# Kernel optimization log

Measured on AMD Instinct MI355X. Metric: run time of the kernel, lower is better.

The kernel has to match this reference:

```python
import jax, jax.numpy as jnp
import numpy as np

N, T, H, KQ, V = 8, 256, 8, 128, 32  # batch, seq (Tq=Tk=T), heads, kq_dim, value_dim(=latent_dim)
SCALE = 1.0 / np.sqrt(KQ)


def setup_inputs() -> dict:
    k = jax.random.split(jax.random.key(0), 10)
    w = 0.05
    return {
        "value": jax.random.normal(k[0], (N, T, V), dtype=jnp.float32),
        "key": jax.random.normal(k[1], (N, T, KQ), dtype=jnp.float32),
        "query": jax.random.normal(k[2], (N, T, KQ), dtype=jnp.float32),
        "mask": jax.random.randint(k[3], (N, T, V), 0, 2, dtype=jnp.int32),
        # attn_linear[0]: query proj, attn_linear[1]: key proj (torch Linear: y = x @ W.T + b)
        "Wq": jax.random.normal(k[4], (H * KQ, KQ), dtype=jnp.float32) * w,
        "bq": jax.random.normal(k[5], (H * KQ,), dtype=jnp.float32) * w,
        "Wk": jax.random.normal(k[6], (H * KQ, KQ), dtype=jnp.float32) * w,
        "bk": jax.random.normal(k[7], (H * KQ,), dtype=jnp.float32) * w,
        "Wo": jax.random.normal(k[8], (V, H * V), dtype=jnp.float32) * w,  # attn_out: Linear(ld*H, ld), ld == V
        "bo": jax.random.normal(k[9], (V,), dtype=jnp.float32) * w,
    }


def reference(value, key, query, mask, Wq, bq, Wk, bk, Wo, bo):
    n, t, vdim = value.shape
    nq, tq, _ = query.shape
    nk, tk, _ = key.shape
    h = Wq.shape[0] // query.shape[-1]
    kq = query.shape[-1]

    # per-head projections: (N, H, T, KQ)
    hq = (query @ Wq.T + bq).reshape(nq, tq, h, kq).transpose(0, 2, 1, 3)
    hk = (key @ Wk.T + bk).reshape(nk, tk, h, kq).transpose(0, 2, 1, 3)

    # scores: (N, H, Tq, Tk), then broadcast per value-dim -> (N, H, Tq, Tk, V)
    scores = jnp.einsum("nhqd,nhkd->nhqk", hq, hk) * jnp.asarray(SCALE, value.dtype)
    scores = jnp.broadcast_to(scores[..., None], (n, h, tq, tk, vdim))

    # mask (N, Tk, V): mask[i,t,d]==0 means value[i,t,d] unobserved
    m = mask[:, None, None, :, :]  # (N,1,1,Tk,V)
    scores = jnp.where(m == 0, jnp.asarray(-1e9, scores.dtype), scores)

    p_attn = jax.nn.softmax(scores, axis=-2)  # softmax over Tk, per value-dim

    # weighted sum over keys: (N, H, Tq, V) -> (N, Tq, H*V)
    out = jnp.einsum("nhqkv,nkv->nqhv", p_attn, value).reshape(n, tq, h * vdim)
    out_rep = out @ Wo.T + bo  # (N, Tq, ld)
    return out_rep, p_attn
```

## Files before the change

### kernel.cpp

```cpp
#include <hip/hip_runtime.h>

#define N_ 8
#define T_ 256
#define H_ 8
#define KQ_ 128
#define V_ 32
#define QT_ 8

typedef float f32x4 __attribute__((ext_vector_type(4)));

__global__ __launch_bounds__(256) void proj_kernel(
    const float* __restrict__ query, const float* __restrict__ key,
    const float* __restrict__ Wq, const float* __restrict__ bq,
    const float* __restrict__ Wk, const float* __restrict__ bk,
    float* __restrict__ hqT, float* __restrict__ hkT)
{
  int b = blockIdx.x;
  int dh = b & 1;
  int tq = (b >> 1) & 3;
  int h  = (b >> 3) & 7;
  int n  = (b >> 6) & 7;
  int proj = b >> 9;
  const float* src  = proj ? key : query;
  const float* W    = proj ? Wk  : Wq;
  const float* bias = proj ? bk  : bq;
  float* dst        = proj ? hkT : hqT;
  int t0 = tq * 64;
  int d0 = dh * 64;

  __shared__ float qs[64 * 132];
  __shared__ float ws[64 * 128];

  {
    const float* qsrc = src + ((size_t)n * T_ + t0) * KQ_;
    const float* wsrc = W + (size_t)(h * KQ_ + d0) * KQ_;
    for (int i = threadIdx.x; i < 64 * 32; i += 256) {
      int r = i >> 5, c4 = (i & 31) * 4;
      *(float4*)&qs[r * 132 + c4] = *(const float4*)&qsrc[(size_t)r * KQ_ + c4];
      *(float4*)&ws[r * 128 + c4] = *(const float4*)&wsrc[(size_t)r * KQ_ + c4];
    }
  }
  __syncthreads();

  int tl   = threadIdx.x & 31;
  int dsub = threadIdx.x >> 5;
  float acc0[8], acc1[8];
#pragma unroll
  for (int dd = 0; dd < 8; ++dd) { acc0[dd] = 0.f; acc1[dd] = 0.f; }

#pragma unroll 4
  for (int j0 = 0; j0 < 128; j0 += 4) {
    float4 q0 = *(const float4*)&qs[tl * 132 + j0];
    float4 q1 = *(const float4*)&qs[(tl + 32) * 132 + j0];
#pragma unroll
    for (int dd = 0; dd < 8; ++dd) {
      float4 w4 = *(const float4*)&ws[(dsub * 8 + dd) * 128 + j0];
      acc0[dd] = fmaf(q0.x, w4.x, acc0[dd]);
      acc0[dd] = fmaf(q0.y, w4.y, acc0[dd]);
      acc0[dd] = fmaf(q0.z, w4.z, acc0[dd]);
      acc0[dd] = fmaf(q0.w, w4.w, acc0[dd]);
      acc1[dd] = fmaf(q1.x, w4.x, acc1[dd]);
      acc1[dd] = fmaf(q1.y, w4.y, acc1[dd]);
      acc1[dd] = fmaf(q1.z, w4.z, acc1[dd]);
      acc1[dd] = fmaf(q1.w, w4.w, acc1[dd]);
    }
  }

#pragma unroll
  for (int dd = 0; dd < 8; ++dd) {
    int d = d0 + dsub * 8 + dd;
    float bb = bias[h * KQ_ + d];
    size_t base = (((size_t)n * H_ + h) * KQ_ + d) * T_ + t0;
    dst[base + tl]      = acc0[dd] + bb;
    dst[base + tl + 32] = acc1[dd] + bb;
  }
}

#define EPAD 9

__global__ __launch_bounds__(256) void attn_kernel(
    const float* __restrict__ hqT, const float* __restrict__ hkT,
    const int* __restrict__ mask, const float* __restrict__ value,
    float* __restrict__ e_ws, float* __restrict__ inv_ws,
    float* __restrict__ out_ws)
{
  const float SCALE = 0.08838834764831845f;
  int b = blockIdx.x;
  int q0 = (b & 31) * QT_;
  int h  = (b >> 5) & 7;
  int n  = b >> 8;
  int t  = threadIdx.x;
  int row0 = (n * H_ + h) * T_ + q0;

  __shared__ float hq_s[KQ_ * 8];
  __shared__ float e_s[T_ * EPAD];
  __shared__ float wred[4 * 8];
  __shared__ float red_s[8 * 8 * 32];
  __shared__ float red_o[8 * 8 * 32];

  const float* hqbase = hqT + ((size_t)n * H_ + h) * KQ_ * T_;
  const float* hkbase = hkT + ((size_t)n * H_ + h) * KQ_ * T_;

  {
    int qq = t & 7, j0 = t >> 3;
#pragma unroll
    for (int rep = 0; rep < 4; ++rep) {
      int j = j0 + rep * 32;
      hq_s[j * 8 + qq] = hqbase[(size_t)j * T_ + q0 + qq];
    }
  }
  __syncthreads();

  float acc[8];
#pragma unroll
  for (int qq = 0; qq < 8; ++qq) acc[qq] = 0.f;
#pragma unroll 4
  for (int j = 0; j < KQ_; ++j) {
    float hk = hkbase[(size_t)j * T_ + t];
    float4 a0 = *(const float4*)&hq_s[j * 8];
    float4 a1 = *(const float4*)&hq_s[j * 8 + 4];
    acc[0] = fmaf(a0.x, hk, acc[0]);
    acc[1] = fmaf(a0.y, hk, acc[1]);
    acc[2] = fmaf(a0.z, hk, acc[2]);
    acc[3] = fmaf(a0.w, hk, acc[3]);
    acc[4] = fmaf(a1.x, hk, acc[4]);
    acc[5] = fmaf(a1.y, hk, acc[5]);
    acc[6] = fmaf(a1.z, hk, acc[6]);
    acc[7] = fmaf(a1.w, hk, acc[7]);
  }
#pragma unroll
  for (int qq = 0; qq < 8; ++qq) acc[qq] *= SCALE;

  float mloc[8];
#pragma unroll
  for (int qq = 0; qq < 8; ++qq) {
    float m = acc[qq];
    for (int off = 32; off >= 1; off >>= 1)
      m = fmaxf(m, __shfl_xor(m, off, 64));
    mloc[qq] = m;
  }
  if ((t & 63) == 0) {
    int w = t >> 6;
#pragma unroll
    for (int qq = 0; qq < 8; ++qq) wred[w * 8 + qq] = mloc[qq];
  }
  __syncthreads();
  {
    float ev[8];
#pragma unroll
    for (int qq = 0; qq < 8; ++qq) {
      float mx = fmaxf(fmaxf(wred[0*8+qq], wred[1*8+qq]),
                       fmaxf(wred[2*8+qq], wred[3*8+qq]));
      ev[qq] = __expf(acc[qq] - mx);
    }
    *(float4*)&e_s[t * EPAD]     = make_float4(ev[0], ev[1], ev[2], ev[3]);
    *(float4*)&e_s[t * EPAD + 4] = make_float4(ev[4], ev[5], ev[6], ev[7]);
#pragma unroll
    for (int qq = 0; qq < 8; ++qq)
      e_ws[(size_t)(row0 + qq) * T_ + t] = ev[qq];
  }
  __syncthreads();

  const int*   mrow = mask  + (size_t)n * T_ * V_;
  const float* vrow = value + (size_t)n * T_ * V_;
  int v = t & 31, kg = t >> 5;
  float s8[8], o8[8];
#pragma unroll
  for (int qq = 0; qq < 8; ++qq) { s8[qq] = 0.f; o8[qq] = 0.f; }
  for (int i = 0; i < 32; ++i) {
    int k = kg * 32 + i;
    float mf = (float)mrow[k * V_ + v];
    float vv = vrow[k * V_ + v];
    float4 e0 = *(const float4*)&e_s[k * EPAD];
    float4 e1 = *(const float4*)&e_s[k * EPAD + 4];
    float p;
    p = e0.x * mf; s8[0] += p; o8[0] = fmaf(p, vv, o8[0]);
    p = e0.y * mf; s8[1] += p; o8[1] = fmaf(p, vv, o8[1]);
    p = e0.z * mf; s8[2] += p; o8[2] = fmaf(p, vv, o8[2]);
    p = e0.w * mf; s8[3] += p; o8[3] = fmaf(p, vv, o8[3]);
    p = e1.x * mf; s8[4] += p; o8[4] = fmaf(p, vv, o8[4]);
    p = e1.y * mf; s8[5] += p; o8[5] = fmaf(p, vv, o8[5]);
    p = e1.z * mf; s8[6] += p; o8[6] = fmaf(p, vv, o8[6]);
    p = e1.w * mf; s8[7] += p; o8[7] = fmaf(p, vv, o8[7]);
  }
#pragma unroll
  for (int qq = 0; qq < 8; ++qq) {
    red_s[(kg * 8 + qq) * 32 + v] = s8[qq];
    red_o[(kg * 8 + qq) * 32 + v] = o8[qq];
  }
  __syncthreads();
  {
    int qq = t >> 5, v2 = t & 31;
    float s = 0.f, o = 0.f;
#pragma unroll
    for (int kg2 = 0; kg2 < 8; ++kg2) {
      s += red_s[(kg2 * 8 + qq) * 32 + v2];
      o += red_o[(kg2 * 8 + qq) * 32 + v2];
    }
    float inv = 1.0f / s;
    inv_ws[(size_t)(row0 + qq) * V_ + v2] = inv;
    out_ws[(((size_t)n * T_ + q0 + qq) * H_ + h) * V_ + v2] = o * inv;
  }
}

__global__ __launch_bounds__(256) void pwrite_kernel(
    const float* __restrict__ e_ws, const float* __restrict__ inv_ws,
    const int* __restrict__ mask, float* __restrict__ p_out)
{
  int b = blockIdx.x;
  int row0 = b * 4;
  int n = row0 >> 11;
  const int* mrow = mask + (size_t)n * T_ * V_;
  int t = threadIdx.x;
  int v0 = (t & 7) * 4;
  int kbase = t >> 3;

  float4 iv[4];
  const float* erow[4];
  f32x4* dst4[4];
#pragma unroll
  for (int qq = 0; qq < 4; ++qq) {
    int row = row0 + qq;
    iv[qq]   = *(const float4*)&inv_ws[(size_t)row * V_ + v0];
    erow[qq] = e_ws + (size_t)row * T_;
    dst4[qq] = (f32x4*)p_out + (size_t)row * 2048;
  }

#pragma unroll
  for (int rep = 0; rep < 8; ++rep) {
    int k = rep * 32 + kbase;
    const int4 m4 = *(const int4*)&mrow[k * V_ + v0];
    float fx = (float)m4.x, fy = (float)m4.y, fz = (float)m4.z, fw = (float)m4.w;
#pragma unroll
    for (int qq = 0; qq < 4; ++qq) {
      float e = erow[qq][k];
      f32x4 pv;
      pv.x = e * fx * iv[qq].x;
      pv.y = e * fy * iv[qq].y;
      pv.z = e * fz * iv[qq].z;
      pv.w = e * fw * iv[qq].w;
      __builtin_nontemporal_store(pv, &dst4[qq][rep * 256 + t]);
    }
  }
}

__global__ __launch_bounds__(256) void outproj_kernel(
    const float* __restrict__ out_ws, const float* __restrict__ Wo,
    const float* __restrict__ bo, float* __restrict__ out_rep)
{
  __shared__ float wot[256 * 33];
  __shared__ float rows_s[4 * 256];
  __shared__ float red[4 * 32];
  int r0 = blockIdx.x * 4;
  for (int i = threadIdx.x; i < 32 * 256; i += 256) {
    int o = i >> 8, c = i & 255;
    wot[c * 33 + o] = Wo[i];
  }
  for (int i = threadIdx.x; i < 4 * 256; i += 256)
    rows_s[i] = out_ws[(size_t)r0 * 256 + i];
  __syncthreads();
  int o  = threadIdx.x & 31;
  int rr = (threadIdx.x >> 5) & 3;
  int kh = threadIdx.x >> 7;
  int cb = kh * 128;
  float acc = 0.f;
#pragma unroll 4
  for (int c = 0; c < 128; ++c)
    acc = fmaf(rows_s[rr * 256 + cb + c], wot[(cb + c) * 33 + o], acc);
  if (kh == 1) red[rr * 32 + o] = acc;
  __syncthreads();
  if (kh == 0)
    out_rep[(size_t)(r0 + rr) * 32 + o] = acc + red[rr * 32 + o] + bo[o];
}

extern "C" void kernel_launch(void* const* d_in, const int* in_sizes, int n_in,
                              void* d_out, int out_size, void* d_ws, size_t ws_size,
                              hipStream_t stream) {
  const float* value = (const float*)d_in[0];
  const float* key   = (const float*)d_in[1];
  const float* query = (const float*)d_in[2];
  const int*   mask  = (const int*)d_in[3];
  const float* Wq = (const float*)d_in[4];
  const float* bq = (const float*)d_in[5];
  const float* Wk = (const float*)d_in[6];
  const float* bk = (const float*)d_in[7];
  const float* Wo = (const float*)d_in[8];
  const float* bo = (const float*)d_in[9];

  float* out_rep = (float*)d_out;
  float* p_out   = (float*)d_out + (size_t)N_ * T_ * V_;

  float* hqT    = (float*)d_ws;
  float* hkT    = hqT    + (size_t)N_ * H_ * KQ_ * T_;
  float* out_ws = hkT    + (size_t)N_ * H_ * KQ_ * T_;
  float* e_ws   = out_ws + (size_t)N_ * T_ * H_ * V_;
  float* inv_ws = e_ws   + (size_t)N_ * H_ * T_ * T_;

  hipLaunchKernelGGL(proj_kernel, dim3(1024), dim3(256), 0, stream,
                     query, key, Wq, bq, Wk, bk, hqT, hkT);
  hipLaunchKernelGGL(attn_kernel, dim3(2048), dim3(256), 0, stream,
                     hqT, hkT, mask, value, e_ws, inv_ws, out_ws);
  hipLaunchKernelGGL(pwrite_kernel, dim3(4096), dim3(256), 0, stream,
                     e_ws, inv_ws, mask, p_out);
  hipLaunchKernelGGL(outproj_kernel, dim3(512), dim3(256), 0, stream,
                     out_ws, Wo, bo, out_rep);
}
```

Before: 170.4 us.

## Retile projection to full sequence per block and shrink attention blocks to one wavefront

The projection kernel now has each block cover all 256 tokens for a 64-wide output slice, looping over K in 32-wide chunks with an 8x8 register tile per thread. This quarters the block count and reuses each weight tile across the whole sequence. The attention kernel now runs one 64-thread wavefront per block, with each lane handling four keys. The softmax max and the final reductions use wave shuffles instead of shared-memory reductions and block barriers. The trade-off is less parallelism: 256 projection blocks and 2048 single-wave attention blocks, plus higher register pressure that may reduce occupancy.

```diff
diff --git a/kernel.cpp b/kernel.cpp
--- a/kernel.cpp
+++ b/kernel.cpp
@@ -5,7 +5,6 @@
 #define H_ 8
 #define KQ_ 128
 #define V_ 32
-#define QT_ 8
 
 typedef float f32x4 __attribute__((ext_vector_type(4)));
 
@@ -17,52 +16,65 @@
 {
   int b = blockIdx.x;
   int dh = b & 1;
-  int tq = (b >> 1) & 3;
-  int h  = (b >> 3) & 7;
-  int n  = (b >> 6) & 7;
-  int proj = b >> 9;
+  int h  = (b >> 1) & 7;
+  int n  = (b >> 4) & 7;
+  int proj = (b >> 7) & 1;
   const float* src  = proj ? key : query;
   const float* W    = proj ? Wk  : Wq;
   const float* bias = proj ? bk  : bq;
   float* dst        = proj ? hkT : hqT;
-  int t0 = tq * 64;
   int d0 = dh * 64;
 
-  __shared__ float qs[64 * 132];
-  __shared__ float ws[64 * 128];
-
-  {
-    const float* qsrc = src + ((size_t)n * T_ + t0) * KQ_;
-    const float* wsrc = W + (size_t)(h * KQ_ + d0) * KQ_;
-    for (int i = threadIdx.x; i < 64 * 32; i += 256) {
-      int r = i >> 5, c4 = (i & 31) * 4;
-      *(float4*)&qs[r * 132 + c4] = *(const float4*)&qsrc[(size_t)r * KQ_ + c4];
-      *(float4*)&ws[r * 128 + c4] = *(const float4*)&wsrc[(size_t)r * KQ_ + c4];
-    }
-  }
-  __syncthreads();
+  __shared__ float qs[256 * 36];
+  __shared__ float ws[64 * 36];
 
   int tl   = threadIdx.x & 31;
   int dsub = threadIdx.x >> 5;
-  float acc0[8], acc1[8];
-#pragma unroll
-  for (int dd = 0; dd < 8; ++dd) { acc0[dd] = 0.f; acc1[dd] = 0.f; }
-
-#pragma unroll 4
-  for (int j0 = 0; j0 < 128; j0 += 4) {
-    float4 q0 = *(const float4*)&qs[tl * 132 + j0];
-    float4 q1 = *(const float4*)&qs[(tl + 32) * 132 + j0];
-#pragma unroll
-    for (int dd = 0; dd < 8; ++dd) {
-      float4 w4 = *(const float4*)&ws[(dsub * 8 + dd) * 128 + j0];
-      acc0[dd] = fmaf(q0.x, w4.x, acc0[dd]);
-      acc0[dd] = fmaf(q0.y, w4.y, acc0[dd]);
-      acc0[dd] = fmaf(q0.z, w4.z, acc0[dd]);
-      acc0[dd] = fmaf(q0.w, w4.w, acc0[dd]);
-      acc1[dd] = fmaf(q1.x, w4.x, acc1[dd]);
-      acc1[dd] = fmaf(q1.y, w4.y, acc1[dd]);
-      acc1[dd] = fmaf(q1.z, w4.z, acc1[dd]);
-      acc1[dd] = fmaf(q1.w, w4.w, acc1[dd]);
+  const float* qsrc = src + (size_t)n * T_ * KQ_;
+  const float* wsrc = W + (size_t)(h * KQ_ + d0) * KQ_;
+
+  float acc[8][8];
+#pragma unroll
+  for (int it = 0; it < 8; ++it)
+#pragma unroll
+    for (int dd = 0; dd < 8; ++dd) acc[it][dd] = 0.f;
+
+  for (int kc = 0; kc < 4; ++kc) {
+    if (kc) __syncthreads();
+    {
+      int r = threadIdx.x >> 3, c4 = (threadIdx.x & 7) * 4;
+#pragma unroll
+      for (int rep = 0; rep < 8; ++rep) {
+        int row = r + rep * 32;
+        *(float4*)&qs[row * 36 + c4] =
+            *(const float4*)&qsrc[(size_t)row * KQ_ + kc * 32 + c4];
+      }
+#pragma unroll
+      for (int rep = 0; rep < 2; ++rep) {
+        int row = r + rep * 32;
+        *(float4*)&ws[row * 36 + c4] =
+            *(const float4*)&wsrc[(size_t)row * KQ_ + kc * 32 + c4];
+      }
+    }
+    __syncthreads();
+
+#pragma unroll 2
+    for (int j0 = 0; j0 < 32; j0 += 4) {
+      float4 qv[8];
+#pragma unroll
+      for (int it = 0; it < 8; ++it)
+        qv[it] = *(const float4*)&qs[(tl + 32 * it) * 36 + j0];
+#pragma unroll
+      for (int dd = 0; dd < 8; ++dd) {
+        float4 w4 = *(const float4*)&ws[(dsub * 8 + dd) * 36 + j0];
+#pragma unroll
+        for (int it = 0; it < 8; ++it) {
+          acc[it][dd] = fmaf(qv[it].x, w4.x, acc[it][dd]);
+          acc[it][dd] = fmaf(qv[it].y, w4.y, acc[it][dd]);
+          acc[it][dd] = fmaf(qv[it].z, w4.z, acc[it][dd]);
+          acc[it][dd] = fmaf(qv[it].w, w4.w, acc[it][dd]);
+        }
+      }
     }
   }
 
@@ -70,15 +82,14 @@
   for (int dd = 0; dd < 8; ++dd) {
     int d = d0 + dsub * 8 + dd;
     float bb = bias[h * KQ_ + d];
-    size_t base = (((size_t)n * H_ + h) * KQ_ + d) * T_ + t0;
-    dst[base + tl]      = acc0[dd] + bb;
-    dst[base + tl + 32] = acc1[dd] + bb;
-  }
-}
-
-#define EPAD 9
-
-__global__ __launch_bounds__(256) void attn_kernel(
+    size_t base = (((size_t)n * H_ + h) * KQ_ + d) * T_;
+#pragma unroll
+    for (int it = 0; it < 8; ++it)
+      dst[base + it * 32 + tl] = acc[it][dd] + bb;
+  }
+}
+
+__global__ __launch_bounds__(64) void attn_kernel(
     const float* __restrict__ hqT, const float* __restrict__ hkT,
     const int* __restrict__ mask, const float* __restrict__ value,
     float* __restrict__ e_ws, float* __restrict__ inv_ws,
@@ -86,93 +97,95 @@
 {
   const float SCALE = 0.08838834764831845f;
   int b = blockIdx.x;
-  int q0 = (b & 31) * QT_;
+  int q0 = (b & 31) * 8;
   int h  = (b >> 5) & 7;
   int n  = b >> 8;
-  int t  = threadIdx.x;
+  int l  = threadIdx.x;
   int row0 = (n * H_ + h) * T_ + q0;
 
-  __shared__ float hq_s[KQ_ * 8];
-  __shared__ float e_s[T_ * EPAD];
-  __shared__ float wred[4 * 8];
-  __shared__ float red_s[8 * 8 * 32];
-  __shared__ float red_o[8 * 8 * 32];
+  __shared__ float hq_s[KQ_ * 12];
+  __shared__ float e_s[T_ * 8];
 
   const float* hqbase = hqT + ((size_t)n * H_ + h) * KQ_ * T_;
   const float* hkbase = hkT + ((size_t)n * H_ + h) * KQ_ * T_;
 
-  {
-    int qq = t & 7, j0 = t >> 3;
-#pragma unroll
-    for (int rep = 0; rep < 4; ++rep) {
-      int j = j0 + rep * 32;
-      hq_s[j * 8 + qq] = hqbase[(size_t)j * T_ + q0 + qq];
-    }
+#pragma unroll
+  for (int rep = 0; rep < 16; ++rep) {
+    int i = l + 64 * rep;
+    int j = i >> 3, qq = i & 7;
+    hq_s[j * 12 + qq] = hqbase[(size_t)j * T_ + q0 + qq];
   }
   __syncthreads();
 
-  float acc[8];
-#pragma unroll
-  for (int qq = 0; qq < 8; ++qq) acc[qq] = 0.f;
+  float acc[4][8];
+#pragma unroll
+  for (int i = 0; i < 4; ++i)
+#pragma unroll
+    for (int qq = 0; qq < 8; ++qq) acc[i][qq] = 0.f;
+
 #pragma unroll 4
   for (int j = 0; j < KQ_; ++j) {
-    float hk = hkbase[(size_t)j * T_ + t];
-    float4 a0 = *(const float4*)&hq_s[j * 8];
-    float4 a1 = *(const float4*)&hq_s[j * 8 + 4];
-    acc[0] = fmaf(a0.x, hk, acc[0]);
-    acc[1] = fmaf(a0.y, hk, acc[1]);
-    acc[2] = fmaf(a0.z, hk, acc[2]);
-    acc[3] = fmaf(a0.w, hk, acc[3]);
-    acc[4] = fmaf(a1.x, hk, acc[4]);
-    acc[5] = fmaf(a1.y, hk, acc[5]);
-    acc[6] = fmaf(a1.z, hk, acc[6]);
-    acc[7] = fmaf(a1.w, hk, acc[7]);
-  }
-#pragma unroll
-  for (int qq = 0; qq < 8; ++qq) acc[qq] *= SCALE;
-
-  float mloc[8];
-#pragma unroll
-  for (int qq = 0; qq < 8; ++qq) {
-    float m = acc[qq];
-    for (int off = 32; off >= 1; off >>= 1)
-      m = fmaxf(m, __shfl_xor(m, off, 64));
-    mloc[qq] = m;
-  }
-  if ((t & 63) == 0) {
-    int w = t >> 6;
-#pragma unroll
-    for (int qq = 0; qq < 8; ++qq) wred[w * 8 + qq] = mloc[qq];
-  }
-  __syncthreads();
+    float hk0 = hkbase[(size_t)j * T_ + l];
+    float hk1 = hkbase[(size_t)j * T_ + l + 64];
+    float hk2 = hkbase[(size_t)j * T_ + l + 128];
+    float hk3 = hkbase[(size_t)j * T_ + l + 192];
+    float4 a0 = *(const float4*)&hq_s[j * 12];
+    float4 a1 = *(const float4*)&hq_s[j * 12 + 4];
+    acc[0][0] = fmaf(a0.x, hk0, acc[0][0]); acc[0][1] = fmaf(a0.y, hk0, acc[0][1]);
+    acc[0][2] = fmaf(a0.z, hk0, acc[0][2]); acc[0][3] = fmaf(a0.w, hk0, acc[0][3]);
+    acc[0][4] = fmaf(a1.x, hk0, acc[0][4]); acc[0][5] = fmaf(a1.y, hk0, acc[0][5]);
+    acc[0][6] = fmaf(a1.z, hk0, acc[0][6]); acc[0][7] = fmaf(a1.w, hk0, acc[0][7]);
+    acc[1][0] = fmaf(a0.x, hk1, acc[1][0]); acc[1][1] = fmaf(a0.y, hk1, acc[1][1]);
+    acc[1][2] = fmaf(a0.z, hk1, acc[1][2]); acc[1][3] = fmaf(a0.w, hk1, acc[1][3]);
+    acc[1][4] = fmaf(a1.x, hk1, acc[1][4]); acc[1][5] = fmaf(a1.y, hk1, acc[1][5]);
+    acc[1][6] = fmaf(a1.z, hk1, acc[1][6]); acc[1][7] = fmaf(a1.w, hk1, acc[1][7]);
+    acc[2][0] = fmaf(a0.x, hk2, acc[2][0]); acc[2][1] = fmaf(a0.y, hk2, acc[2][1]);
+    acc[2][2] = fmaf(a0.z, hk2, acc[2][2]); acc[2][3] = fmaf(a0.w, hk2, acc[2][3]);
+    acc[2][4] = fmaf(a1.x, hk2, acc[2][4]); acc[2][5] = fmaf(a1.y, hk2, acc[2][5]);
+    acc[2][6] = fmaf(a1.z, hk2, acc[2][6]); acc[2][7] = fmaf(a1.w, hk2, acc[2][7]);
+    acc[3][0] = fmaf(a0.x, hk3, acc[3][0]); acc[3][1] = fmaf(a0.y, hk3, acc[3][1]);
+    acc[3][2] = fmaf(a0.z, hk3, acc[3][2]); acc[3][3] = fmaf(a0.w, hk3, acc[3][3]);
+    acc[3][4] = fmaf(a1.x, hk3, acc[3][4]); acc[3][5] = fmaf(a1.y, hk3, acc[3][5]);
+    acc[3][6] = fmaf(a1.z, hk3, acc[3][6]); acc[3][7] = fmaf(a1.w, hk3, acc[3][7]);
+  }
+
+  float ev[4][8];
   {
-    float ev[8];
 #pragma unroll
     for (int qq = 0; qq < 8; ++qq) {
-      float mx = fmaxf(fmaxf(wred[0*8+qq], wred[1*8+qq]),
-                       fmaxf(wred[2*8+qq], wred[3*8+qq]));
-      ev[qq] = __expf(acc[qq] - mx);
-    }
-    *(float4*)&e_s[t * EPAD]     = make_float4(ev[0], ev[1], ev[2], ev[3]);
-    *(float4*)&e_s[t * EPAD + 4] = make_float4(ev[4], ev[5], ev[6], ev[7]);
+      float m = fmaxf(fmaxf(acc[0][qq] * SCALE, acc[1][qq] * SCALE),
+                      fmaxf(acc[2][qq] * SCALE, acc[3][qq] * SCALE));
+      for (int off = 32; off >= 1; off >>= 1)
+        m = fmaxf(m, __shfl_xor(m, off, 64));
+#pragma unroll
+      for (int i = 0; i < 4; ++i)
+        ev[i][qq] = __expf(acc[i][qq] * SCALE - m);
+    }
+  }
+#pragma unroll
+  for (int i = 0; i < 4; ++i) {
 #pragma unroll
     for (int qq = 0; qq < 8; ++qq)
-      e_ws[(size_t)(row0 + qq) * T_ + t] = ev[qq];
+      e_ws[(size_t)(row0 + qq) * T_ + l + 64 * i] = ev[i][qq];
+    int k = l + 64 * i;
+    *(f32x4*)&e_s[k * 8]     = f32x4{ev[i][0], ev[i][1], ev[i][2], ev[i][3]};
+    *(f32x4*)&e_s[k * 8 + 4] = f32x4{ev[i][4], ev[i][5], ev[i][6], ev[i][7]};
   }
   __syncthreads();
 
   const int*   mrow = mask  + (size_t)n * T_ * V_;
   const float* vrow = value + (size_t)n * T_ * V_;
-  int v = t & 31, kg = t >> 5;
+  int v = l & 31, kh = l >> 5;
   float s8[8], o8[8];
 #pragma unroll
   for (int qq = 0; qq < 8; ++qq) { s8[qq] = 0.f; o8[qq] = 0.f; }
-  for (int i = 0; i < 32; ++i) {
-    int k = kg * 32 + i;
+#pragma unroll 4
+  for (int i = 0; i < 128; ++i) {
+    int k = kh * 128 + i;
     float mf = (float)mrow[k * V_ + v];
     float vv = vrow[k * V_ + v];
-    float4 e0 = *(const float4*)&e_s[k * EPAD];
-    float4 e1 = *(const float4*)&e_s[k * EPAD + 4];
+    float4 e0 = *(const float4*)&e_s[k * 8];
+    float4 e1 = *(const float4*)&e_s[k * 8 + 4];
     float p;
     p = e0.x * mf; s8[0] += p; o8[0] = fmaf(p, vv, o8[0]);
     p = e0.y * mf; s8[1] += p; o8[1] = fmaf(p, vv, o8[1]);
@@ -185,21 +198,16 @@
   }
 #pragma unroll
   for (int qq = 0; qq < 8; ++qq) {
-    red_s[(kg * 8 + qq) * 32 + v] = s8[qq];
-    red_o[(kg * 8 + qq) * 32 + v] = o8[qq];
-  }
-  __syncthreads();
-  {
-    int qq = t >> 5, v2 = t & 31;
-    float s = 0.f, o = 0.f;
-#pragma unroll
-    for (int kg2 = 0; kg2 < 8; ++kg2) {
-      s += red_s[(kg2 * 8 + qq) * 32 + v2];
-      o += red_o[(kg2 * 8 + qq) * 32 + v2];
-    }
-    float inv = 1.0f / s;
-    inv_ws[(size_t)(row0 + qq) * V_ + v2] = inv;
-    out_ws[(((size_t)n * T_ + q0 + qq) * H_ + h) * V_ + v2] = o * inv;
+    s8[qq] += __shfl_xor(s8[qq], 32, 64);
+    o8[qq] += __shfl_xor(o8[qq], 32, 64);
+  }
+  if (kh == 0) {
+#pragma unroll
+    for (int qq = 0; qq < 8; ++qq) {
+      float inv = 1.0f / s8[qq];
+      inv_ws[(size_t)(row0 + qq) * V_ + v] = inv;
+      out_ws[(((size_t)n * T_ + q0 + qq) * H_ + h) * V_ + v] = o8[qq] * inv;
+    }
   }
 }
 
@@ -296,9 +304,9 @@
   float* e_ws   = out_ws + (size_t)N_ * T_ * H_ * V_;
   float* inv_ws = e_ws   + (size_t)N_ * H_ * T_ * T_;
 
-  hipLaunchKernelGGL(proj_kernel, dim3(1024), dim3(256), 0, stream,
+  hipLaunchKernelGGL(proj_kernel, dim3(256), dim3(256), 0, stream,
                      query, key, Wq, bq, Wk, bk, hqT, hkT);
-  hipLaunchKernelGGL(attn_kernel, dim3(2048), dim3(256), 0, stream,
+  hipLaunchKernelGGL(attn_kernel, dim3(2048), dim3(64), 0, stream,
                      hqT, hkT, mask, value, e_ws, inv_ws, out_ws);
   hipLaunchKernelGGL(pwrite_kernel, dim3(4096), dim3(256), 0, stream,
                      e_ws, inv_ws, mask, p_out);
```

After: 170.4 us. Within noise of the previous version (+0.0%).
